# Performance work log

Hardware: AMD Instinct MI355X
Metric: run time of the kernel (lower is better)

Reference implementation:

```python
import jax, jax.numpy as jnp
import numpy as np

E = 96   # embed dim (MultiheadAttention(96, 6))
H = 6    # heads
DH = E // H  # head dim = 16


def setup_inputs() -> dict:
    key = jax.random.key(0)
    ks = jax.random.split(key, 6)
    N, G = 4096, 64
    feats = jax.random.normal(ks[0], (N, E), jnp.float32)
    group = jax.random.randint(ks[1], (N,), 0, G)
    s = 1.0 / np.sqrt(E)
    # nn.MultiheadAttention packed in_proj [3E, E] and out_proj [E, E]
    w_in = jax.random.uniform(ks[2], (3 * E, E), jnp.float32, -s, s)
    b_in = jnp.zeros((3 * E,), jnp.float32)
    w_out = jax.random.uniform(ks[3], (E, E), jnp.float32, -s, s)
    b_out = jnp.zeros((E,), jnp.float32)
    # classifier Linear(96, 1)
    w_cls = jax.random.uniform(ks[4], (1, E), jnp.float32, -s, s)
    b_cls = jnp.zeros((1,), jnp.float32)
    return {"feats": feats, "group": group, "w_in": w_in, "b_in": b_in,
            "w_out": w_out, "b_out": b_out, "w_cls": w_cls, "b_cls": b_cls}


def reference(feats, group, w_in, b_in, w_out, b_out, w_cls, b_cls):
    # Per-group self-attention: softmax restricted to rows of the same group
    # is mathematically identical to running MHA on each group separately.
    N = feats.shape[0]
    qkv = feats @ w_in.T + b_in                     # [N, 3E]
    q, k, v = jnp.split(qkv, 3, axis=-1)            # each [N, E]
    to_heads = lambda t: t.reshape(N, H, DH).transpose(1, 0, 2)  # [H, N, DH]
    q = to_heads(q) * (1.0 / np.sqrt(DH))
    k = to_heads(k)
    v = to_heads(v)
    scores = jnp.einsum('hnd,hmd->hnm', q, k)       # [H, N, N]
    same_group = group[:, None] == group[None, :]   # [N, N] (diag always True)
    scores = jnp.where(same_group[None], scores, jnp.float32(-1e9))
    attn = jax.nn.softmax(scores, axis=-1)
    out = jnp.einsum('hnm,hmd->hnd', attn, v)       # [H, N, DH]
    out = out.transpose(1, 0, 2).reshape(N, E)
    out = out @ w_out.T + b_out                     # out_proj
    logits = out @ w_cls.T + b_cls                  # [N, 1]
    return jax.nn.sigmoid(logits)[:, 0]             # cluster_scores [N]
```

## Files before the change

kernel.cpp:

```cpp
#include <hip/hip_runtime.h>
#include <math.h>

#define N 4096
#define E 96
#define H 6
#define DH 16
#define G 64
#define CMAX 128
#define KSTR 19
#define FSTR 104
#define NW 8
#define NT 512

typedef __attribute__((ext_vector_type(8))) short short8;
typedef __attribute__((ext_vector_type(4))) float f32x4;

static __device__ __forceinline__ unsigned short f2bf(float f) {
    unsigned u = __builtin_bit_cast(unsigned, f);
    return (unsigned short)((u + 0x7fffu + ((u >> 16) & 1u)) >> 16);
}
static __device__ __forceinline__ unsigned pack2(float lo, float hi) {
    return (unsigned)f2bf(lo) | ((unsigned)f2bf(hi) << 16);
}

__global__ __launch_bounds__(NT, 4) void fused_kernel(const float* __restrict__ feats,
                                                      const int* __restrict__ grp,
                                                      const float* __restrict__ w_in,
                                                      const float* __restrict__ b_in,
                                                      const float* __restrict__ w_out,
                                                      const float* __restrict__ w_cls,
                                                      float* __restrict__ part) {
    __shared__ short fA[CMAX * FSTR];
    __shared__ short wB[48 * FSTR];
    __shared__ float bia[48];
    __shared__ float kh[CMAX * KSTR];
    __shared__ float vh[CMAX * KSTR];
    __shared__ float qh[64 * KSTR];
    __shared__ float ps[NW * CMAX];
    __shared__ int   bucket[CMAX];
    __shared__ unsigned long long smask[64];
    __shared__ int   scount[64];
    __shared__ int   soffs[64];
    __shared__ float wfh[DH];
    __shared__ int   scnt;

    int g  = blockIdx.x & 63;
    int hh = blockIdx.x >> 6;
    int h  = hh >> 1;
    int hb = hh & 1;
    int tid = threadIdx.x, lane = tid & 63, wv = tid >> 6;

    #pragma unroll
    for (int c8 = 0; c8 < 8; ++c8) {
        int cc = wv * 8 + c8;
        bool mt = (grp[(cc << 6) + lane] == g);
        unsigned long long mask = __ballot(mt);
        if (lane == 0) { smask[cc] = mask; scount[cc] = __popcll(mask); }
    }

    if (tid < 384) {
        int row = tid >> 3, seg = tid & 7;
        int gcol = (row >> 4) * E + h * DH + (row & 15);
        const float4* src = (const float4*)(w_in + gcol * E + seg * 12);
        unsigned* dst = (unsigned*)(wB + row * FSTR + seg * 12);
        #pragma unroll
        for (int t = 0; t < 3; ++t) {
            float4 v = src[t];
            dst[2 * t]     = pack2(v.x, v.y);
            dst[2 * t + 1] = pack2(v.z, v.w);
        }
    } else if (tid < 432) {
        int c = tid - 384;
        bia[c] = b_in[(c >> 4) * E + h * DH + (c & 15)];
    } else if (wv == 7) {
        int dd = lane & 15, u4 = lane >> 4;
        float s = 0.f;
        for (int u = u4 * 24; u < u4 * 24 + 24; ++u)
            s += w_cls[u] * w_out[u * E + h * DH + dd];
        s += __shfl_xor(s, 16, 64);
        s += __shfl_xor(s, 32, 64);
        if (lane < DH) wfh[lane] = s;
    }
    __syncthreads();

    if (wv == 0) {
        int v = scount[lane];
        int x = v;
        #pragma unroll
        for (int o = 1; o < 64; o <<= 1) {
            int y = __shfl_up(x, o, 64);
            if (lane >= o) x += y;
        }
        soffs[lane] = x - v;
        if (lane == 63) scnt = x;
    } else {
        for (int idx = tid - 64; idx < CMAX * KSTR; idx += NT - 64) vh[idx] = 0.f;
    }
    __syncthreads();

    int cnt = scnt; if (cnt > CMAX) cnt = CMAX;

    #pragma unroll
    for (int c8 = 0; c8 < 8; ++c8) {
        int cc = wv * 8 + c8;
        unsigned long long mask = smask[cc];
        if ((mask >> lane) & 1ULL) {
            int pos = soffs[cc] + __popcll(mask & ((1ULL << lane) - 1ULL));
            if (pos < CMAX) bucket[pos] = (cc << 6) + lane;
        }
    }
    __syncthreads();

    {
        int srow = tid >> 2, sq = tid & 3;
        if (srow < cnt) {
            const float4* src = (const float4*)(feats + bucket[srow] * E + sq * 24);
            unsigned* dst = (unsigned*)(fA + srow * FSTR + sq * 24);
            #pragma unroll
            for (int t = 0; t < 6; ++t) {
                float4 v = src[t];
                dst[2 * t]     = pack2(v.x, v.y);
                dst[2 * t + 1] = pack2(v.z, v.w);
            }
        }
    }
    __syncthreads();

    {
        int lr = lane & 15, kg = lane >> 4;
        int njobs = ((cnt + 15) >> 4) * 3;
        for (int jj = wv; jj < njobs; jj += NW) {
            int rt = jj / 3;
            int ct = jj - rt * 3;
            const short* ab = fA + (rt * 16 + lr) * FSTR + kg * 8;
            const short* bb = wB + (ct * 16 + lr) * FSTR + kg * 8;
            f32x4 acc = {0.f, 0.f, 0.f, 0.f};
            acc = __builtin_amdgcn_mfma_f32_16x16x32_bf16(*(const short8*)(ab),
                                                          *(const short8*)(bb), acc, 0, 0, 0);
            acc = __builtin_amdgcn_mfma_f32_16x16x32_bf16(*(const short8*)(ab + 32),
                                                          *(const short8*)(bb + 32), acc, 0, 0, 0);
            acc = __builtin_amdgcn_mfma_f32_16x16x32_bf16(*(const short8*)(ab + 64),
                                                          *(const short8*)(bb + 64), acc, 0, 0, 0);
            float bias = bia[ct * 16 + lr];
            #pragma unroll
            for (int r = 0; r < 4; ++r) {
                int row = rt * 16 + kg * 4 + r;
                if (row < cnt) {
                    float v = acc[r] + bias;
                    if (ct == 1)      kh[row * KSTR + lr] = v;
                    else if (ct == 2) vh[row * KSTR + lr] = v;
                    else if ((row & 1) == hb) qh[(row >> 1) * KSTR + lr] = v * 0.25f;
                }
            }
        }
    }
    __syncthreads();

    for (int j = wv; 2 * j + hb < cnt; j += NW) {
        int r = 2 * j + hb;
        float qv[16];
        #pragma unroll
        for (int e = 0; e < 16; ++e) qv[e] = qh[j * KSTR + e];

        float a0 = 0.f;
        #pragma unroll
        for (int e = 0; e < 16; ++e) a0 += qv[e] * kh[lane * KSTR + e];
        float s0 = (lane < cnt) ? a0 : -INFINITY;
        float s1 = -INFINITY;
        if (cnt > 64) {
            float a1 = 0.f;
            #pragma unroll
            for (int e = 0; e < 16; ++e) a1 += qv[e] * kh[(64 + lane) * KSTR + e];
            s1 = (64 + lane < cnt) ? a1 : -INFINITY;
        }

        float m = fmaxf(s0, s1);
        #pragma unroll
        for (int o = 32; o >= 1; o >>= 1) m = fmaxf(m, __shfl_xor(m, o, 64));
        float p0 = __expf(s0 - m);
        float p1 = (cnt > 64) ? __expf(s1 - m) : 0.f;
        float l = p0 + p1;
        #pragma unroll
        for (int o = 32; o >= 1; o >>= 1) l += __shfl_xor(l, o, 64);
        ps[wv * CMAX + lane] = p0;
        ps[wv * CMAX + 64 + lane] = p1;

        int mm4 = lane >> 4, dd = lane & 15;
        float acc = 0.f;
        #pragma unroll
        for (int k = 0; k < 16; ++k) {
            int m2 = mm4 + 4 * k;
            acc += ps[wv * CMAX + m2] * vh[m2 * KSTR + dd];
        }
        if (cnt > 64) {
            #pragma unroll
            for (int k = 16; k < 32; ++k) {
                int m2 = mm4 + 4 * k;
                acc += ps[wv * CMAX + m2] * vh[m2 * KSTR + dd];
            }
        }
        acc += __shfl_xor(acc, 16, 64);
        acc += __shfl_xor(acc, 32, 64);

        float pt = (acc / l) * wfh[dd];
        pt += __shfl_xor(pt, 1, 64);
        pt += __shfl_xor(pt, 2, 64);
        pt += __shfl_xor(pt, 4, 64);
        pt += __shfl_xor(pt, 8, 64);
        if (lane == 0) part[bucket[r] * 8 + h] = pt;
    }
}

__global__ __launch_bounds__(512) void sigmoid_kernel(const float* __restrict__ part,
                                                      const float* __restrict__ w_cls,
                                                      const float* __restrict__ b_out,
                                                      const float* __restrict__ b_cls,
                                                      float* __restrict__ out) {
    __shared__ float sbias;
    int tid = threadIdx.x;
    if (tid < 64) {
        float s = w_cls[tid] * b_out[tid];
        if (tid < 32) s += w_cls[tid + 64] * b_out[tid + 64];
        #pragma unroll
        for (int o = 32; o >= 1; o >>= 1) s += __shfl_xor(s, o, 64);
        if (tid == 0) sbias = s + b_cls[0];
    }
    __syncthreads();
    int i = blockIdx.x * 512 + tid;
    const float4* p = (const float4*)(part + i * 8);
    float4 u = p[0], v = p[1];
    float s = u.x + u.y + u.z + u.w + v.x + v.y + sbias;
    out[i] = 1.f / (1.f + __expf(-s));
}

extern "C" void kernel_launch(void* const* d_in, const int* in_sizes, int n_in,
                              void* d_out, int out_size, void* d_ws, size_t ws_size,
                              hipStream_t stream) {
    const float* feats = (const float*)d_in[0];
    const int*   grp   = (const int*)  d_in[1];
    const float* w_in  = (const float*)d_in[2];
    const float* b_in  = (const float*)d_in[3];
    const float* w_out = (const float*)d_in[4];
    const float* b_out = (const float*)d_in[5];
    const float* w_cls = (const float*)d_in[6];
    const float* b_cls = (const float*)d_in[7];
    float* out = (float*)d_out;

    float* part = (float*)d_ws;

    fused_kernel<<<G * H * 2, NT, 0, stream>>>(feats, grp, w_in, b_in, w_out, w_cls, part);
    sigmoid_kernel<<<N / 512, 512, 0, stream>>>(part, w_cls, b_out, b_cls, out);
}
```

Before: 100.6 us.

## Merge row-half blocks and process two query rows per wave iteration

Each block now handles all query rows of a (group, head) pair instead of splitting rows by parity across two blocks. This halves the grid and removes the duplicated feature load, K/V projection and mask setup. Each wave now processes two query rows per iteration, sharing K and V shared-memory reads across both rows for more ILP. The trade-off is fewer blocks (384) to spread over the CUs, and more registers and LDS per block, which may reduce occupancy.

```diff
diff --git a/kernel.cpp b/kernel.cpp
--- a/kernel.cpp
+++ b/kernel.cpp
@@ -35,8 +35,8 @@
     __shared__ float bia[48];
     __shared__ float kh[CMAX * KSTR];
     __shared__ float vh[CMAX * KSTR];
-    __shared__ float qh[64 * KSTR];
-    __shared__ float ps[NW * CMAX];
+    __shared__ float qh[CMAX * KSTR];
+    __shared__ float ps[NW * 2 * CMAX];
     __shared__ int   bucket[CMAX];
     __shared__ unsigned long long smask[64];
     __shared__ int   scount[64];
@@ -44,10 +44,8 @@
     __shared__ float wfh[DH];
     __shared__ int   scnt;
 
-    int g  = blockIdx.x & 63;
-    int hh = blockIdx.x >> 6;
-    int h  = hh >> 1;
-    int hb = hh & 1;
+    int g = blockIdx.x & 63;
+    int h = blockIdx.x >> 6;
     int tid = threadIdx.x, lane = tid & 63, wv = tid >> 6;
 
     #pragma unroll
@@ -149,65 +147,98 @@
                     float v = acc[r] + bias;
                     if (ct == 1)      kh[row * KSTR + lr] = v;
                     else if (ct == 2) vh[row * KSTR + lr] = v;
-                    else if ((row & 1) == hb) qh[(row >> 1) * KSTR + lr] = v * 0.25f;
+                    else              qh[row * KSTR + lr] = v * 0.25f;
                 }
             }
         }
     }
     __syncthreads();
 
-    for (int j = wv; 2 * j + hb < cnt; j += NW) {
-        int r = 2 * j + hb;
-        float qv[16];
-        #pragma unroll
-        for (int e = 0; e < 16; ++e) qv[e] = qh[j * KSTR + e];
-
-        float a0 = 0.f;
-        #pragma unroll
-        for (int e = 0; e < 16; ++e) a0 += qv[e] * kh[lane * KSTR + e];
-        float s0 = (lane < cnt) ? a0 : -INFINITY;
-        float s1 = -INFINITY;
+    float* ps0 = ps + (2 * wv) * CMAX;
+    float* ps1 = ps + (2 * wv + 1) * CMAX;
+    for (int j0 = wv; j0 < cnt; j0 += 2 * NW) {
+        int j1 = j0 + NW;
+        bool has1 = (j1 < cnt);
+        int j1r = has1 ? j1 : j0;
+
+        float qv0[16], qv1[16];
+        #pragma unroll
+        for (int e = 0; e < 16; ++e) {
+            qv0[e] = qh[j0 * KSTR + e];
+            qv1[e] = qh[j1r * KSTR + e];
+        }
+
+        float a00 = 0.f, a10 = 0.f;
+        #pragma unroll
+        for (int e = 0; e < 16; ++e) {
+            float kl = kh[lane * KSTR + e];
+            a00 += qv0[e] * kl;
+            a10 += qv1[e] * kl;
+        }
+        float s00 = (lane < cnt) ? a00 : -INFINITY;
+        float s10 = (lane < cnt) ? a10 : -INFINITY;
+        float s01 = -INFINITY, s11 = -INFINITY;
         if (cnt > 64) {
-            float a1 = 0.f;
-            #pragma unroll
-            for (int e = 0; e < 16; ++e) a1 += qv[e] * kh[(64 + lane) * KSTR + e];
-            s1 = (64 + lane < cnt) ? a1 : -INFINITY;
-        }
-
-        float m = fmaxf(s0, s1);
-        #pragma unroll
-        for (int o = 32; o >= 1; o >>= 1) m = fmaxf(m, __shfl_xor(m, o, 64));
-        float p0 = __expf(s0 - m);
-        float p1 = (cnt > 64) ? __expf(s1 - m) : 0.f;
-        float l = p0 + p1;
-        #pragma unroll
-        for (int o = 32; o >= 1; o >>= 1) l += __shfl_xor(l, o, 64);
-        ps[wv * CMAX + lane] = p0;
-        ps[wv * CMAX + 64 + lane] = p1;
+            float a01 = 0.f, a11 = 0.f;
+            #pragma unroll
+            for (int e = 0; e < 16; ++e) {
+                float kl = kh[(64 + lane) * KSTR + e];
+                a01 += qv0[e] * kl;
+                a11 += qv1[e] * kl;
+            }
+            s01 = (64 + lane < cnt) ? a01 : -INFINITY;
+            s11 = (64 + lane < cnt) ? a11 : -INFINITY;
+        }
+
+        float m0 = fmaxf(s00, s01), m1 = fmaxf(s10, s11);
+        #pragma unroll
+        for (int o = 32; o >= 1; o >>= 1) {
+            m0 = fmaxf(m0, __shfl_xor(m0, o, 64));
+            m1 = fmaxf(m1, __shfl_xor(m1, o, 64));
+        }
+        float p00 = __expf(s00 - m0), p10 = __expf(s10 - m1);
+        float p01 = (cnt > 64) ? __expf(s01 - m0) : 0.f;
+        float p11 = (cnt > 64) ? __expf(s11 - m1) : 0.f;
+        float l0 = p00 + p01, l1 = p10 + p11;
+        #pragma unroll
+        for (int o = 32; o >= 1; o >>= 1) {
+            l0 += __shfl_xor(l0, o, 64);
+            l1 += __shfl_xor(l1, o, 64);
+        }
+        ps0[lane] = p00; ps0[64 + lane] = p01;
+        ps1[lane] = p10; ps1[64 + lane] = p11;
 
         int mm4 = lane >> 4, dd = lane & 15;
-        float acc = 0.f;
+        float acc0 = 0.f, acc1 = 0.f;
         #pragma unroll
         for (int k = 0; k < 16; ++k) {
             int m2 = mm4 + 4 * k;
-            acc += ps[wv * CMAX + m2] * vh[m2 * KSTR + dd];
+            float vv = vh[m2 * KSTR + dd];
+            acc0 += ps0[m2] * vv;
+            acc1 += ps1[m2] * vv;
         }
         if (cnt > 64) {
             #pragma unroll
             for (int k = 16; k < 32; ++k) {
                 int m2 = mm4 + 4 * k;
-                acc += ps[wv * CMAX + m2] * vh[m2 * KSTR + dd];
-            }
-        }
-        acc += __shfl_xor(acc, 16, 64);
-        acc += __shfl_xor(acc, 32, 64);
-
-        float pt = (acc / l) * wfh[dd];
-        pt += __shfl_xor(pt, 1, 64);
-        pt += __shfl_xor(pt, 2, 64);
-        pt += __shfl_xor(pt, 4, 64);
-        pt += __shfl_xor(pt, 8, 64);
-        if (lane == 0) part[bucket[r] * 8 + h] = pt;
+                float vv = vh[m2 * KSTR + dd];
+                acc0 += ps0[m2] * vv;
+                acc1 += ps1[m2] * vv;
+            }
+        }
+        acc0 += __shfl_xor(acc0, 16, 64); acc1 += __shfl_xor(acc1, 16, 64);
+        acc0 += __shfl_xor(acc0, 32, 64); acc1 += __shfl_xor(acc1, 32, 64);
+
+        float pt0 = (acc0 / l0) * wfh[dd];
+        float pt1 = (acc1 / l1) * wfh[dd];
+        pt0 += __shfl_xor(pt0, 1, 64);  pt1 += __shfl_xor(pt1, 1, 64);
+        pt0 += __shfl_xor(pt0, 2, 64);  pt1 += __shfl_xor(pt1, 2, 64);
+        pt0 += __shfl_xor(pt0, 4, 64);  pt1 += __shfl_xor(pt1, 4, 64);
+        pt0 += __shfl_xor(pt0, 8, 64);  pt1 += __shfl_xor(pt1, 8, 64);
+        if (lane == 0) {
+            part[bucket[j0] * 8 + h] = pt0;
+            if (has1) part[bucket[j1] * 8 + h] = pt1;
+        }
     }
 }
 
@@ -248,6 +279,6 @@
 
     float* part = (float*)d_ws;
 
-    fused_kernel<<<G * H * 2, NT, 0, stream>>>(feats, grp, w_in, b_in, w_out, w_cls, part);
+    fused_kernel<<<G * H, NT, 0, stream>>>(feats, grp, w_in, b_in, w_out, w_cls, part);
     sigmoid_kernel<<<N / 512, 512, 0, stream>>>(part, w_cls, b_out, b_cls, out);
 }
```

New measurement: 101.1 us. Within noise of the previous version (+0.5%).
